# Kernel optimization log

Measured on AMD Instinct MI355X. Metric: run time of the kernel, lower is better.

The kernel has to match this reference:

```python
import jax, jax.numpy as jnp
import numpy as np

B, S, D, E, K = 4, 2048, 1024, 8, 2
H = 4 * D  # expert hidden dim


def setup_inputs() -> dict:
    key = jax.random.key(0)
    ks = jax.random.split(key, 4)
    sc = lambda n: 1.0 / np.sqrt(n)
    return {
        "x": jax.random.normal(ks[0], (B, S, D), jnp.float32),
        "gate_w": jax.random.normal(ks[1], (D, E), jnp.float32) * sc(D),
        "gate_b": jnp.zeros((E,), jnp.float32),
        "w1": jax.random.normal(ks[2], (E, D, H), jnp.float32) * sc(D),
        "b1": jnp.zeros((E, H), jnp.float32),
        "w2": jax.random.normal(ks[3], (E, H, D), jnp.float32) * sc(H),
        "b2": jnp.zeros((E, D), jnp.float32),
    }


def reference(x, gate_w, gate_b, w1, b1, w2, b2):
    Bx, Sx, Dx = x.shape
    n_exp = w1.shape[0]

    # --- TopKRouter: softmax over expert logits, keep top-k scores at their slots ---
    logits = jnp.einsum('bsd,de->bse', x, gate_w) + gate_b          # [B,S,E]
    scores = jax.nn.softmax(logits, axis=-1)
    topk_s, topk_i = jax.lax.top_k(scores, K)                        # [B,S,K]
    onehot = jax.nn.one_hot(topk_i, n_exp, dtype=scores.dtype)       # [B,S,K,E]
    dispatch = jnp.einsum('bske,bsk->bse', onehot, topk_s)           # [B,S,E]

    # --- DynamicMoE combine ---
    xf = x.reshape(-1, Dx)                                           # [B*S, D]
    wf = dispatch.reshape(-1, n_exp)                                 # [B*S, E]
    out = jnp.zeros_like(xf)
    for i in range(n_exp):  # fixed small expert count; sequential overwrite semantics
        wi = wf[:, i:i + 1]                                          # [B*S, 1]
        # routing weight multiplies the expert INPUT (as in the original)
        h = jax.nn.relu((xf * wi) @ w1[i] + b1[i])                   # [B*S, 4D]
        y = h @ w2[i] + b2[i]                                        # [B*S, D]
        # out[mask] = y : later experts overwrite earlier ones
        out = jnp.where(wi > 0, y, out)
    return out.reshape(Bx, Sx, Dx)
```

## Files before the change

### kernel.cpp

```cpp
#include <hip/hip_runtime.h>
#include <hip/hip_bf16.h>
#include <stdint.h>

typedef __attribute__((ext_vector_type(8))) __bf16 bf16x8;
typedef __attribute__((ext_vector_type(4))) __bf16 bf16x4;
typedef __attribute__((ext_vector_type(4))) float  f32x4;

#define NTOK   8192
#define DMODEL 1024
#define HDIM   4096
#define NEXP   8

__device__ __forceinline__ void glds16(const void* g, void* l) {
  __builtin_amdgcn_global_load_lds(
      (const __attribute__((address_space(1))) uint32_t*)g,
      (__attribute__((address_space(3))) uint32_t*)l, 16, 0, 0);
}

#define WAITV(N) asm volatile("s_waitcnt vmcnt(" #N ")" ::: "memory")
#define SBAR()  do { __builtin_amdgcn_sched_barrier(0); \
                     __builtin_amdgcn_s_barrier();      \
                     __builtin_amdgcn_sched_barrier(0); } while (0)

__global__ void zero_cnt_kernel(int* cnt) {
  if (threadIdx.x < NEXP) cnt[threadIdx.x] = 0;
}

__global__ void prefix_kernel(const int* __restrict__ cnt, int* __restrict__ base) {
  if (threadIdx.x == 0) {
    int b = 0;
    base[0] = 0;
    for (int e = 0; e < NEXP; ++e) {
      b += (cnt[e] + 255) & ~255;
      base[e + 1] = b;
    }
  }
}

__global__ __launch_bounds__(256) void moe_gate_kernel(
    const float* __restrict__ x, const float* __restrict__ gw,
    const float* __restrict__ gb, float* __restrict__ wgt,
    int* __restrict__ cnt, int* __restrict__ meta)
{
  const int lane = threadIdx.x & 63;
  const int wv   = threadIdx.x >> 6;
  const int t    = (blockIdx.x << 2) + wv;
  const float* xp = x + (size_t)t * DMODEL;

  float acc[NEXP];
#pragma unroll
  for (int e = 0; e < NEXP; ++e) acc[e] = 0.f;

#pragma unroll
  for (int j = 0; j < DMODEL / 64; ++j) {
    const int d = (j << 6) + lane;
    const float xv = xp[d];
    const float4 g0 = *(const float4*)(gw + (size_t)d * NEXP);
    const float4 g1 = *(const float4*)(gw + (size_t)d * NEXP + 4);
    acc[0] = fmaf(xv, g0.x, acc[0]);
    acc[1] = fmaf(xv, g0.y, acc[1]);
    acc[2] = fmaf(xv, g0.z, acc[2]);
    acc[3] = fmaf(xv, g0.w, acc[3]);
    acc[4] = fmaf(xv, g1.x, acc[4]);
    acc[5] = fmaf(xv, g1.y, acc[5]);
    acc[6] = fmaf(xv, g1.z, acc[6]);
    acc[7] = fmaf(xv, g1.w, acc[7]);
  }
#pragma unroll
  for (int e = 0; e < NEXP; ++e) {
#pragma unroll
    for (int off = 32; off > 0; off >>= 1)
      acc[e] += __shfl_xor(acc[e], off, 64);
  }
  if (lane == 0) {
    float l[NEXP];
#pragma unroll
    for (int e = 0; e < NEXP; ++e) l[e] = acc[e] + gb[e];
    int i1 = 0; float m1 = l[0];
#pragma unroll
    for (int e = 1; e < NEXP; ++e) if (l[e] > m1) { m1 = l[e]; i1 = e; }
    int i2 = -1; float m2 = -3.402823466e38f;
#pragma unroll
    for (int e = 0; e < NEXP; ++e) if (e != i1 && l[e] > m2) { m2 = l[e]; i2 = e; }
    const int es = i1 > i2 ? i1 : i2;
    float s = 0.f;
#pragma unroll
    for (int e = 0; e < NEXP; ++e) s += expf(l[e] - m1);
    const float w = expf(l[es] - m1) / s;
    wgt[t] = w;
    const int pos = atomicAdd(&cnt[es], 1);
    meta[t] = (es << 13) | pos;
  }
}

__global__ __launch_bounds__(256) void pack_x_kernel(
    const float* __restrict__ x, const float* __restrict__ wgt,
    const int* __restrict__ meta, const int* __restrict__ base,
    __bf16* __restrict__ xbf, int* __restrict__ sortmap)
{
  const int t = blockIdx.x * 2 + (threadIdx.x >> 7);
  const int l = threadIdx.x & 127;
  const int m = meta[t];
  const int es = m >> 13, pos = m & 8191;
  const int dst = base[es] + pos;
  const float w = wgt[t];
  const float4 a = *(const float4*)(x + (size_t)t * DMODEL + l * 8);
  const float4 b = *(const float4*)(x + (size_t)t * DMODEL + l * 8 + 4);
  bf16x8 o;
  o[0] = (__bf16)(a.x * w); o[1] = (__bf16)(a.y * w);
  o[2] = (__bf16)(a.z * w); o[3] = (__bf16)(a.w * w);
  o[4] = (__bf16)(b.x * w); o[5] = (__bf16)(b.y * w);
  o[6] = (__bf16)(b.z * w); o[7] = (__bf16)(b.w * w);
  *(bf16x8*)(xbf + (size_t)dst * DMODEL + l * 8) = o;
  if (l == 0) sortmap[dst] = t;
}

__global__ __launch_bounds__(256) void zeropad_kernel(
    const int* __restrict__ cnt, const int* __restrict__ base,
    __bf16* __restrict__ xbf)
{
  const int e = blockIdx.x;
  const int c0 = cnt[e], cp = base[e + 1] - base[e];
  bf16x4 z; z[0] = z[1] = z[2] = z[3] = (__bf16)0.f;
  for (int r = c0; r < cp; ++r)
    *(bf16x4*)(xbf + (size_t)(base[e] + r) * DMODEL + threadIdx.x * 4) = z;
}

template<int N, int K>
__global__ __launch_bounds__(256) void pack_w_kernel(
    const float* __restrict__ src, __bf16* __restrict__ dst)
{
  const int k0 = blockIdx.x * 64, np = blockIdx.y, e = blockIdx.z;
  const int t = threadIdx.x;
  __shared__ __bf16 sh[8192];

  const float* sp = src + (size_t)e * K * N + (size_t)k0 * N + np * 128;
#pragma unroll
  for (int i = 0; i < 8; ++i) {
    const int id = i * 256 + t;
    const int k = id >> 5, n4 = id & 31;
    const float4 v = *(const float4*)(sp + (size_t)k * N + n4 * 4);
    const int phys = n4 ^ ((k & 3) << 3);
    bf16x4 o; o[0] = (__bf16)v.x; o[1] = (__bf16)v.y;
              o[2] = (__bf16)v.z; o[3] = (__bf16)v.w;
    *(bf16x4*)&sh[k * 128 + phys * 4] = o;
  }
  __syncthreads();

  __bf16* dbase = dst + ((size_t)(e * (N / 128) + np) * 128) * K + k0;
#pragma unroll
  for (int j2 = 0; j2 < 4; ++j2) {
    const int c = j2 * 256 + t;
    const int n = c >> 3, ks8 = c & 7;
    bf16x8 v;
#pragma unroll
    for (int j = 0; j < 8; ++j) {
      const int k = ks8 * 8 + j;
      v[j] = sh[k * 128 + (((n >> 2) ^ ((k & 3) << 3)) << 2) + (n & 3)];
    }
    *(bf16x8*)(dbase + (size_t)n * K + ks8 * 8) = v;
  }
}

template<int KSTEPS, int ASTRIDE, int NOUT, bool RELU, bool SCATTER, typename OutT>
__global__ __launch_bounds__(512, 1) void moe_gemm256_kernel(
    const __bf16* __restrict__ Am, const __bf16* __restrict__ Bp,
    const float* __restrict__ bias, const int* __restrict__ cnt,
    const int* __restrict__ base, const int* __restrict__ sortmap,
    OutT* __restrict__ outp)
{
  const int e  = blockIdx.z;
  const int ce = cnt[e];
  const int rb = base[e];
  const int cep = base[e + 1] - rb;
  const int m0 = blockIdx.y << 8;
  if (m0 >= cep) return;
  const int np = blockIdx.x, n0 = np << 8;

  const int tid = threadIdx.x, lane = tid & 63, wv = tid >> 6;
  const int wm = wv >> 2, wn = wv & 3;
  const int rl = lane & 15, sl = lane >> 4;

  __shared__ alignas(16) __bf16 lds[65536];

  const __bf16* asrc[4];
  const __bf16* bsrc[4];
#pragma unroll
  for (int i = 0; i < 4; ++i) {
    const int c = (wv * 4 + i) * 64 + lane;
    const int r = c >> 3, p = c & 7;
    const int koff = (p ^ (r & 7)) * 8;
    asrc[i] = Am + (size_t)(rb + m0 + r) * ASTRIDE + koff;
    bsrc[i] = Bp + ((size_t)(e * (NOUT / 128) + np * 2) * 128 + r) * ASTRIDE + koff;
  }

  auto stage = [&](int buf, int ks) {
    __bf16* Ad = lds + buf * 32768;
    __bf16* Bd = Ad + 16384;
#pragma unroll
    for (int i = 0; i < 4; ++i)
      glds16(asrc[i] + ks * 64, Ad + (wv * 4 + i) * 512);
#pragma unroll
    for (int i = 0; i < 4; ++i)
      glds16(bsrc[i] + ks * 64, Bd + (wv * 4 + i) * 512);
  };

  f32x4 acc[8][4] = {};

  stage(0, 0);
  for (int ks = 0; ks < KSTEPS; ++ks) {
    const int buf = ks & 1;
    WAITV(0);
    SBAR();
    if (ks + 1 < KSTEPS) stage(buf ^ 1, ks + 1);

    const char* Ab = (const char*)lds + buf * 65536 + wm * 16384;
    const char* Bb = (const char*)lds + buf * 65536 + 32768 + (wn >> 1) * 16384;

#pragma unroll
    for (int kk = 0; kk < 2; ++kk) {
      bf16x8 af[8];
#pragma unroll
      for (int mf = 0; mf < 8; ++mf) {
        const int row = mf * 16 + rl;
        af[mf] = *(const bf16x8*)(Ab + row * 128 + (((kk * 4 + sl) ^ (row & 7)) << 4));
      }
#pragma unroll
      for (int nh = 0; nh < 2; ++nh) {
        bf16x8 bf[2];
#pragma unroll
        for (int nf2 = 0; nf2 < 2; ++nf2) {
          const int row = (wn & 1) * 64 + nh * 32 + nf2 * 16 + rl;
          bf[nf2] = *(const bf16x8*)(Bb + row * 128 + (((kk * 4 + sl) ^ (row & 7)) << 4));
        }
        __builtin_amdgcn_s_setprio(1);
#pragma unroll
        for (int mf = 0; mf < 8; ++mf)
#pragma unroll
          for (int nf2 = 0; nf2 < 2; ++nf2)
            acc[mf][nh * 2 + nf2] = __builtin_amdgcn_mfma_f32_16x16x32_bf16(
                af[mf], bf[nf2], acc[mf][nh * 2 + nf2], 0, 0, 0);
        __builtin_amdgcn_s_setprio(0);
      }
    }
  }

  const int cl = rl;
  float bb[4];
#pragma unroll
  for (int nf = 0; nf < 4; ++nf)
    bb[nf] = bias[(size_t)e * NOUT + n0 + wn * 64 + nf * 16 + cl];

#pragma unroll
  for (int mf = 0; mf < 8; ++mf) {
#pragma unroll
    for (int j = 0; j < 4; ++j) {
      const int gm = m0 + wm * 128 + mf * 16 + sl * 4 + j;
      if constexpr (SCATTER) {
        if (gm < ce) {
          const int tok = sortmap[rb + gm];
          OutT* op = outp + (size_t)tok * NOUT + n0 + wn * 64;
#pragma unroll
          for (int nf = 0; nf < 4; ++nf)
            op[nf * 16 + cl] = (OutT)(acc[mf][nf][j] + bb[nf]);
        }
      } else {
        OutT* op = outp + (size_t)(rb + gm) * NOUT + n0 + wn * 64;
        const bool live = gm < ce;
#pragma unroll
        for (int nf = 0; nf < 4; ++nf) {
          float v = acc[mf][nf][j] + bb[nf];
          if constexpr (RELU) v = fmaxf(v, 0.f);
          op[nf * 16 + cl] = live ? (OutT)v : (OutT)0.f;
        }
      }
    }
  }
}

extern "C" void kernel_launch(void* const* d_in, const int* in_sizes, int n_in,
                              void* d_out, int out_size, void* d_ws, size_t ws_size,
                              hipStream_t stream)
{
  const float* x  = (const float*)d_in[0];
  const float* gw = (const float*)d_in[1];
  const float* gb = (const float*)d_in[2];
  const float* w1 = (const float*)d_in[3];
  const float* b1 = (const float*)d_in[4];
  const float* w2 = (const float*)d_in[5];
  const float* b2 = (const float*)d_in[6];
  float* out = (float*)d_out;

  char* ws = (char*)d_ws;
  int*    cnt     = (int*)ws;
  int*    base    = (int*)(ws + 256);
  int*    meta    = (int*)(ws + 4096);
  float*  wgt     = (float*)(ws + 40960);
  int*    sortmap = (int*)(ws + 81920);
  __bf16* xbf     = (__bf16*)(ws + ((size_t)1   << 20));
  __bf16* hmat    = (__bf16*)(ws + ((size_t)22  << 20));
  __bf16* wp      = (__bf16*)(ws + ((size_t)104 << 20));

  zero_cnt_kernel<<<1, 64, 0, stream>>>(cnt);
  moe_gate_kernel<<<NTOK / 4, 256, 0, stream>>>(x, gw, gb, wgt, cnt, meta);
  prefix_kernel<<<1, 64, 0, stream>>>(cnt, base);
  pack_x_kernel<<<NTOK / 2, 256, 0, stream>>>(x, wgt, meta, base, xbf, sortmap);
  zeropad_kernel<<<NEXP, 256, 0, stream>>>(cnt, base, xbf);

  pack_w_kernel<HDIM, DMODEL><<<dim3(DMODEL / 64, HDIM / 128, NEXP), 256, 0, stream>>>(w1, wp);
  moe_gemm256_kernel<DMODEL / 64, DMODEL, HDIM, true, false, __bf16>
      <<<dim3(HDIM / 256, 40, NEXP), 512, 0, stream>>>(
          xbf, wp, b1, cnt, base, sortmap, hmat);

  pack_w_kernel<DMODEL, HDIM><<<dim3(HDIM / 64, DMODEL / 128, NEXP), 256, 0, stream>>>(w2, wp);
  moe_gemm256_kernel<HDIM / 64, HDIM, DMODEL, false, true, float>
      <<<dim3(DMODEL / 256, 40, NEXP), 512, 0, stream>>>(
          hmat, wp, b2, cnt, base, sortmap, out);
}
```

Before: 417.8 us.

## Use 4-stage K=32 LDS pipeline with tile-contiguous packed weight layout

The K step per stage drops from 64 to 32, and the double-buffered LDS loop becomes a four-buffer ring with three stages in flight, using partial vmcnt waits. The weight pack kernel now writes each 256xK32 B tile as one contiguous 16 KB block, so B loads become linear streams. The LDS swizzle is changed to match the shorter 64-byte rows. The aim is to hide global-load latency better at the same LDS footprint, at the cost of twice as many barriers per K and less MFMA work between syncs.

```diff
diff --git a/kernel.cpp b/kernel.cpp
--- a/kernel.cpp
+++ b/kernel.cpp
@@ -147,18 +147,22 @@
   }
   __syncthreads();
 
-  __bf16* dbase = dst + ((size_t)(e * (N / 128) + np) * 128) * K + k0;
+  const int np2 = np >> 1, nh = np & 1;
 #pragma unroll
   for (int j2 = 0; j2 < 4; ++j2) {
-    const int c = j2 * 256 + t;
-    const int n = c >> 3, ks8 = c & 7;
+    const int idx = j2 * 256 + t;
+    const int ksl = idx >> 9, rem = idx & 511;
+    const int rloc = rem >> 2, p = rem & 3;
+    const int rglob = nh * 128 + rloc;
     bf16x8 v;
 #pragma unroll
     for (int j = 0; j < 8; ++j) {
-      const int k = ks8 * 8 + j;
-      v[j] = sh[k * 128 + (((n >> 2) ^ ((k & 3) << 3)) << 2) + (n & 3)];
-    }
-    *(bf16x8*)(dbase + (size_t)n * K + ks8 * 8) = v;
+      const int k = ksl * 32 + ((p ^ (rglob & 3)) << 3) + j;
+      v[j] = sh[k * 128 + (((rloc >> 2) ^ ((k & 3) << 3)) << 2) + (rloc & 3)];
+    }
+    __bf16* dp = dst + (((size_t)e * (N / 256) + np2) * (K / 32) + (k0 >> 5) + ksl) * 8192
+                     + ((size_t)(nh * 512 + rem)) * 8;
+    *(bf16x8*)dp = v;
   }
 }
 
@@ -183,66 +187,63 @@
 
   __shared__ alignas(16) __bf16 lds[65536];
 
-  const __bf16* asrc[4];
-  const __bf16* bsrc[4];
-#pragma unroll
-  for (int i = 0; i < 4; ++i) {
-    const int c = (wv * 4 + i) * 64 + lane;
-    const int r = c >> 3, p = c & 7;
-    const int koff = (p ^ (r & 7)) * 8;
+  const __bf16* asrc[2];
+  const __bf16* bsrc[2];
+#pragma unroll
+  for (int i = 0; i < 2; ++i) {
+    const int c = (wv * 2 + i) * 64 + lane;
+    const int r = c >> 2, p = c & 3;
+    const int koff = ((p ^ (r & 3)) << 3);
     asrc[i] = Am + (size_t)(rb + m0 + r) * ASTRIDE + koff;
-    bsrc[i] = Bp + ((size_t)(e * (NOUT / 128) + np * 2) * 128 + r) * ASTRIDE + koff;
+    bsrc[i] = Bp + ((size_t)e * (NOUT / 256) + np) * (size_t)KSTEPS * 8192
+                 + (size_t)c * 8;
   }
 
   auto stage = [&](int buf, int ks) {
-    __bf16* Ad = lds + buf * 32768;
-    __bf16* Bd = Ad + 16384;
-#pragma unroll
-    for (int i = 0; i < 4; ++i)
-      glds16(asrc[i] + ks * 64, Ad + (wv * 4 + i) * 512);
-#pragma unroll
-    for (int i = 0; i < 4; ++i)
-      glds16(bsrc[i] + ks * 64, Bd + (wv * 4 + i) * 512);
+    __bf16* Ad = lds + buf * 16384;
+    __bf16* Bd = Ad + 8192;
+#pragma unroll
+    for (int i = 0; i < 2; ++i)
+      glds16(asrc[i] + ks * 32, Ad + (wv * 2 + i) * 512);
+#pragma unroll
+    for (int i = 0; i < 2; ++i)
+      glds16(bsrc[i] + (size_t)ks * 8192, Bd + (wv * 2 + i) * 512);
   };
 
   f32x4 acc[8][4] = {};
 
-  stage(0, 0);
+  auto compute = [&](int buf) {
+    const char* Ab = (const char*)lds + buf * 32768 + wm * 8192;
+    const char* Bb = (const char*)lds + buf * 32768 + 16384;
+    bf16x8 af[8], bf[4];
+#pragma unroll
+    for (int mf = 0; mf < 8; ++mf) {
+      const int row = mf * 16 + rl;
+      af[mf] = *(const bf16x8*)(Ab + row * 64 + (((sl ^ (row & 3))) << 4));
+    }
+#pragma unroll
+    for (int nf = 0; nf < 4; ++nf) {
+      const int row = wn * 64 + nf * 16 + rl;
+      bf[nf] = *(const bf16x8*)(Bb + row * 64 + (((sl ^ (row & 3))) << 4));
+    }
+    __builtin_amdgcn_s_setprio(1);
+#pragma unroll
+    for (int nf = 0; nf < 4; ++nf)
+#pragma unroll
+      for (int mf = 0; mf < 8; ++mf)
+        acc[mf][nf] = __builtin_amdgcn_mfma_f32_16x16x32_bf16(
+            af[mf], bf[nf], acc[mf][nf], 0, 0, 0);
+    __builtin_amdgcn_s_setprio(0);
+  };
+
+  stage(0, 0); stage(1, 1); stage(2, 2);
   for (int ks = 0; ks < KSTEPS; ++ks) {
-    const int buf = ks & 1;
-    WAITV(0);
+    if (ks + 2 < KSTEPS)      WAITV(8);
+    else if (ks + 1 < KSTEPS) WAITV(4);
+    else                      WAITV(0);
     SBAR();
-    if (ks + 1 < KSTEPS) stage(buf ^ 1, ks + 1);
-
-    const char* Ab = (const char*)lds + buf * 65536 + wm * 16384;
-    const char* Bb = (const char*)lds + buf * 65536 + 32768 + (wn >> 1) * 16384;
-
-#pragma unroll
-    for (int kk = 0; kk < 2; ++kk) {
-      bf16x8 af[8];
-#pragma unroll
-      for (int mf = 0; mf < 8; ++mf) {
-        const int row = mf * 16 + rl;
-        af[mf] = *(const bf16x8*)(Ab + row * 128 + (((kk * 4 + sl) ^ (row & 7)) << 4));
-      }
-#pragma unroll
-      for (int nh = 0; nh < 2; ++nh) {
-        bf16x8 bf[2];
-#pragma unroll
-        for (int nf2 = 0; nf2 < 2; ++nf2) {
-          const int row = (wn & 1) * 64 + nh * 32 + nf2 * 16 + rl;
-          bf[nf2] = *(const bf16x8*)(Bb + row * 128 + (((kk * 4 + sl) ^ (row & 7)) << 4));
-        }
-        __builtin_amdgcn_s_setprio(1);
-#pragma unroll
-        for (int mf = 0; mf < 8; ++mf)
-#pragma unroll
-          for (int nf2 = 0; nf2 < 2; ++nf2)
-            acc[mf][nh * 2 + nf2] = __builtin_amdgcn_mfma_f32_16x16x32_bf16(
-                af[mf], bf[nf2], acc[mf][nh * 2 + nf2], 0, 0, 0);
-        __builtin_amdgcn_s_setprio(0);
-      }
-    }
+    if (ks + 3 < KSTEPS) stage((ks + 3) & 3, ks + 3);
+    compute(ks & 3);
   }
 
   const int cl = rl;
@@ -255,7 +256,7 @@
   for (int mf = 0; mf < 8; ++mf) {
 #pragma unroll
     for (int j = 0; j < 4; ++j) {
-      const int gm = m0 + wm * 128 + mf * 16 + sl * 4 + j;
+      const int gm = m0 + wm * 128 + mf * 16 + ((lane >> 4) << 2) + j;
       if constexpr (SCATTER) {
         if (gm < ce) {
           const int tok = sortmap[rb + gm];
@@ -308,12 +309,12 @@
   zeropad_kernel<<<NEXP, 256, 0, stream>>>(cnt, base, xbf);
 
   pack_w_kernel<HDIM, DMODEL><<<dim3(DMODEL / 64, HDIM / 128, NEXP), 256, 0, stream>>>(w1, wp);
-  moe_gemm256_kernel<DMODEL / 64, DMODEL, HDIM, true, false, __bf16>
+  moe_gemm256_kernel<DMODEL / 32, DMODEL, HDIM, true, false, __bf16>
       <<<dim3(HDIM / 256, 40, NEXP), 512, 0, stream>>>(
           xbf, wp, b1, cnt, base, sortmap, hmat);
 
   pack_w_kernel<DMODEL, HDIM><<<dim3(HDIM / 64, DMODEL / 128, NEXP), 256, 0, stream>>>(w2, wp);
-  moe_gemm256_kernel<HDIM / 64, HDIM, DMODEL, false, true, float>
+  moe_gemm256_kernel<HDIM / 32, HDIM, DMODEL, false, true, float>
       <<<dim3(DMODEL / 256, 40, NEXP), 512, 0, stream>>>(
           hmat, wp, b2, cnt, base, sortmap, out);
 }
```

New measurement: 423.5 us. Within noise of the previous version (+1.4%).
